# Optimization experiments

Hardware: AMD Instinct MI355X
Metric: run time of the kernel (lower is better)

## Reference

```python
import jax, jax.numpy as jnp
import numpy as np

D_MODEL, SEQ, D_HEAD, N_HEAD, D_MLP = 1024, 2048, 64, 16, 4096
BATCH = 2
LN_EPS = 1e-5


def layer_norm(x, gamma, beta):
    mu = jnp.mean(x, axis=-1, keepdims=True)
    var = jnp.mean(jnp.square(x - mu), axis=-1, keepdims=True)
    return (x - mu) * jax.lax.rsqrt(var + LN_EPS) * gamma + beta


def setup_inputs() -> dict:
    key = jax.random.key(0)
    ks = jax.random.split(key, 10)
    s = 1.0 / np.sqrt(D_MODEL)
    x = jax.random.normal(ks[0], (BATCH, SEQ, D_MODEL), dtype=jnp.float32)
    # per-head Q/K/V projections, stacked: [H, d_model, d_head]
    wq = jax.random.uniform(ks[1], (N_HEAD, D_MODEL, D_HEAD), jnp.float32, -s, s)
    wk = jax.random.uniform(ks[2], (N_HEAD, D_MODEL, D_HEAD), jnp.float32, -s, s)
    wv = jax.random.uniform(ks[3], (N_HEAD, D_MODEL, D_HEAD), jnp.float32, -s, s)
    wo = jax.random.uniform(ks[4], (N_HEAD * D_HEAD, D_MODEL), jnp.float32, -s, s)
    sm = 1.0 / np.sqrt(D_MLP)
    w_in = jax.random.uniform(ks[5], (D_MODEL, D_MLP), jnp.float32, -s, s)
    b_in = jax.random.uniform(ks[6], (D_MLP,), jnp.float32, -s, s)
    w_out = jax.random.uniform(ks[7], (D_MLP, D_MODEL), jnp.float32, -sm, sm)
    b_out = jax.random.uniform(ks[8], (D_MODEL,), jnp.float32, -sm, sm)
    g1 = jnp.ones((D_MODEL,), jnp.float32)
    bt1 = jnp.zeros((D_MODEL,), jnp.float32)
    g2 = jnp.ones((D_MODEL,), jnp.float32)
    bt2 = jnp.zeros((D_MODEL,), jnp.float32)
    return {"x": x, "wq": wq, "wk": wk, "wv": wv, "wo": wo,
            "w_in": w_in, "b_in": b_in, "w_out": w_out, "b_out": b_out,
            "g1": g1, "bt1": bt1, "g2": g2, "bt2": bt2}


def reference(x, wq, wk, wv, wo, w_in, b_in, w_out, b_out, g1, bt1, g2, bt2):
    B, S, D = x.shape
    # multi-head attention (all heads batched)
    q = jnp.einsum('bsd,hde->bhse', x, wq)  # [B,H,S,dh]
    k = jnp.einsum('bsd,hde->bhse', x, wk)
    v = jnp.einsum('bsd,hde->bhse', x, wv)
    scores = jnp.einsum('bhie,bhje->bhij', q, k) / np.sqrt(D_HEAD)
    causal = jnp.tril(jnp.ones((S, S), dtype=bool))
    scores = jnp.where(causal, scores, -jnp.inf)
    attn = jax.nn.softmax(scores, axis=-1)
    head_out = jnp.einsum('bhij,bhje->bhie', attn, v)  # [B,H,S,dh]
    # concat heads in order (head 0 first) -> [B,S,H*dh]
    head_out = jnp.transpose(head_out, (0, 2, 1, 3)).reshape(B, S, N_HEAD * D_HEAD)
    x = x + layer_norm(head_out @ wo, g1, bt1)
    mlp = jax.nn.relu(x @ w_in + b_in) @ w_out + b_out
    x = x + layer_norm(mlp, g2, bt2)
    return x
```

## Files before the change

### kernel.cpp

```cpp
#include <hip/hip_runtime.h>
#include <hip/hip_bf16.h>
#include <math.h>

#define DM 1024
#define SEQ 2048
#define DH 64
#define NH 16
#define DMLP 4096
#define BATCH 2
#define ROWS (BATCH*SEQ)

typedef __attribute__((ext_vector_type(4))) float f32x4;
typedef __attribute__((ext_vector_type(8))) short bf16x8;

__device__ __forceinline__ void gl2lds16(const __hip_bfloat16* g, __hip_bfloat16* l) {
  __builtin_amdgcn_global_load_lds(
      (const __attribute__((address_space(1))) void*)g,
      (__attribute__((address_space(3))) void*)l, 16, 0, 0);
}

template<int K, int OUT_BF16, int BIAS, int RELU>
__global__ __launch_bounds__(512) void gemm256(
    const __hip_bfloat16* __restrict__ A,
    const __hip_bfloat16* __restrict__ BT,
    float* __restrict__ Cf,
    __hip_bfloat16* __restrict__ Cb,
    const float* __restrict__ bias,
    int N)
{
  constexpr int NT = K / 64;
  __shared__ __align__(16) __hip_bfloat16 As[2][16384];
  __shared__ __align__(16) __hip_bfloat16 Bs[2][16384];
  const int t    = threadIdx.x;
  const int wave = t >> 6;
  const int lane = t & 63;
  const int col  = lane & 15;
  const int quad = lane >> 4;
  const int m0 = blockIdx.x * 256;
  const int n0 = blockIdx.y * 256;
  const int wm = (wave >> 2) * 128;
  const int wn = (wave & 3) * 64;

  const int tr = t >> 3;
  const int tc = (t & 7) ^ (tr & 7);
  const __hip_bfloat16* gA = A  + (size_t)(m0 + tr) * K + tc * 8;
  const __hip_bfloat16* gB = BT + (size_t)(n0 + tr) * K + tc * 8;

  const int sw  = col & 7;
  const int ao0 = ((quad)     ^ sw) * 8;
  const int ao1 = ((4 + quad) ^ sw) * 8;

  f32x4 acc[8][4] = {};

#define STAGE_A(h, u) do {                                                     \
    gl2lds16(gA + (size_t)(h)*128*K + (u)*64,                                  \
             &As[(u)&1][(h)*8192 + wave*512]);                                 \
    gl2lds16(gA + (size_t)(h)*128*K + (u)*64 + (size_t)64*K,                   \
             &As[(u)&1][(h)*8192 + 4096 + wave*512]);                          \
  } while (0)
#define STAGE_B(h, u) do {                                                     \
    gl2lds16(gB + (size_t)(h)*128*K + (u)*64,                                  \
             &Bs[(u)&1][(h)*8192 + wave*512]);                                 \
    gl2lds16(gB + (size_t)(h)*128*K + (u)*64 + (size_t)64*K,                   \
             &Bs[(u)&1][(h)*8192 + 4096 + wave*512]);                          \
  } while (0)
#define LOAD_A(base) do { _Pragma("unroll")                                    \
    for (int i = 0; i < 4; ++i) {                                              \
      af[i][0] = *(const bf16x8*)(pA + (base) + i*1024 + ao0);                 \
      af[i][1] = *(const bf16x8*)(pA + (base) + i*1024 + ao1);                 \
    } } while (0)
#define LOAD_BX(arr, base) do { _Pragma("unroll")                              \
    for (int j = 0; j < 2; ++j) {                                              \
      arr[j][0] = *(const bf16x8*)(pB + (base) + j*1024 + ao0);                \
      arr[j][1] = *(const bf16x8*)(pB + (base) + j*1024 + ao1);                \
    } } while (0)
#define PHASE_TAIL(MB, NB, BARR) do {                                          \
    asm volatile("s_barrier" ::: "memory");                                    \
    asm volatile("s_waitcnt lgkmcnt(0)" ::: "memory");                         \
    __builtin_amdgcn_s_setprio(1);                                             \
    _Pragma("unroll")                                                          \
    for (int kk = 0; kk < 2; ++kk)                                             \
      _Pragma("unroll")                                                        \
      for (int i = 0; i < 4; ++i)                                              \
        _Pragma("unroll")                                                      \
        for (int j = 0; j < 2; ++j)                                            \
          acc[(MB)+i][(NB)+j] = __builtin_amdgcn_mfma_f32_16x16x32_bf16(       \
              af[i][kk], BARR[j][kk], acc[(MB)+i][(NB)+j], 0, 0, 0);           \
    __builtin_amdgcn_s_setprio(0);                                             \
    asm volatile("s_barrier" ::: "memory");                                    \
  } while (0)

  STAGE_A(0, 0); STAGE_B(0, 0); STAGE_A(1, 0); STAGE_B(1, 0);
  if (NT > 1) {
    STAGE_A(0, 1); STAGE_B(0, 1); STAGE_A(1, 1); STAGE_B(1, 1);
    asm volatile("s_waitcnt vmcnt(8)" ::: "memory");
  } else {
    asm volatile("s_waitcnt vmcnt(0)" ::: "memory");
  }
  asm volatile("s_barrier" ::: "memory");

  #pragma unroll 2
  for (int u = 0; u < NT; ++u) {
    const __hip_bfloat16* pA = As[u & 1] + (wm + col) * 64;
    const __hip_bfloat16* pB = Bs[u & 1] + (wn + col) * 64;
    const bool s2 = (u + 2 < NT);
    bf16x8 af[4][2], bl[2][2], bh[2][2];

    LOAD_A(0);
    LOAD_BX(bl, 0);
    PHASE_TAIL(0, 0, bl);

    LOAD_BX(bh, 2048);
    PHASE_TAIL(0, 2, bh);

    LOAD_A(4096);
    if (s2) { STAGE_B(0, u + 2); STAGE_B(1, u + 2); }
    PHASE_TAIL(4, 2, bh);

    if (s2) {
      STAGE_A(0, u + 2); STAGE_A(1, u + 2);
      asm volatile("s_waitcnt vmcnt(8)" ::: "memory");
    } else {
      asm volatile("s_waitcnt vmcnt(0)" ::: "memory");
    }
    PHASE_TAIL(4, 0, bl);
  }
#undef STAGE_A
#undef STAGE_B
#undef LOAD_A
#undef LOAD_BX
#undef PHASE_TAIL

  #pragma unroll
  for (int mi = 0; mi < 8; ++mi) {
    #pragma unroll
    for (int ni = 0; ni < 4; ++ni) {
      const int cn = n0 + wn + ni*16 + col;
      float bv = 0.f;
      if (BIAS) bv = bias[cn];
      #pragma unroll
      for (int r = 0; r < 4; ++r) {
        const int cm = m0 + wm + mi*16 + quad*4 + r;
        float v = acc[mi][ni][r];
        if (BIAS) v += bv;
        if (RELU) v = fmaxf(v, 0.f);
        if (OUT_BF16) Cb[(size_t)cm * N + cn] = __float2bfloat16(v);
        else          Cf[(size_t)cm * N + cn] = v;
      }
    }
  }
}

template<int KS>
__global__ __launch_bounds__(512) void gemm256x128(
    const __hip_bfloat16* __restrict__ A,
    const __hip_bfloat16* __restrict__ BT,
    float* __restrict__ Cf,
    int N, int K, long long zstride)
{
  constexpr int NT = KS / 64;
  static_assert(NT >= 2, "pipeline needs >=2 K-tiles");
  __shared__ __align__(16) __hip_bfloat16 As[2][16384];
  __shared__ __align__(16) __hip_bfloat16 Bs[2][8192];
  const int t    = threadIdx.x;
  const int wave = t >> 6;
  const int lane = t & 63;
  const int col  = lane & 15;
  const int quad = lane >> 4;
  const int m0 = blockIdx.x * 256;
  const int n0 = blockIdx.y * 128;
  const int kz = (int)blockIdx.z * KS;
  const int wm = (wave >> 1) * 64;
  const int wn = (wave & 1) * 64;

  const int tr = t >> 3;
  const int tc = (t & 7) ^ (tr & 7);
  const __hip_bfloat16* gA = A  + (size_t)(m0 + tr) * K + kz + tc * 8;
  const __hip_bfloat16* gB = BT + (size_t)(n0 + tr) * K + kz + tc * 8;

  const int sw  = col & 7;
  const int ao0 = ((quad)     ^ sw) * 8;
  const int ao1 = ((4 + quad) ^ sw) * 8;

  f32x4 acc[4][4] = {};

#define SA(u) do { _Pragma("unroll")                                           \
    for (int q = 0; q < 4; ++q)                                                \
      gl2lds16(gA + (size_t)(q*64)*K + (u)*64,                                 \
               &As[(u)&1][q*4096 + wave*512]);                                 \
  } while (0)
#define SB(u) do { _Pragma("unroll")                                           \
    for (int q = 0; q < 2; ++q)                                                \
      gl2lds16(gB + (size_t)(q*64)*K + (u)*64,                                 \
               &Bs[(u)&1][q*4096 + wave*512]);                                 \
  } while (0)

  SA(0); SB(0); SA(1);

  #pragma unroll 2
  for (int v = 0; v < NT; ++v) {
    const __hip_bfloat16* pA = As[v & 1] + (wm + col) * 64;
    const __hip_bfloat16* pB = Bs[v & 1] + (wn + col) * 64;
    bf16x8 af[4][2], bf[4][2];

    if (v + 1 < NT) {
      SB(v + 1);
      asm volatile("s_waitcnt vmcnt(6)" ::: "memory");
    } else {
      asm volatile("s_waitcnt vmcnt(0)" ::: "memory");
    }
    asm volatile("s_barrier" ::: "memory");
    #pragma unroll
    for (int i = 0; i < 4; ++i) {
      af[i][0] = *(const bf16x8*)(pA + i*1024 + ao0);
      af[i][1] = *(const bf16x8*)(pA + i*1024 + ao1);
    }
    #pragma unroll
    for (int j = 0; j < 2; ++j) {
      bf[j][0] = *(const bf16x8*)(pB + j*1024 + ao0);
      bf[j][1] = *(const bf16x8*)(pB + j*1024 + ao1);
    }
    asm volatile("s_waitcnt lgkmcnt(0)" ::: "memory");
    __builtin_amdgcn_s_setprio(1);
    #pragma unroll
    for (int kk = 0; kk < 2; ++kk)
      #pragma unroll
      for (int i = 0; i < 4; ++i)
        #pragma unroll
        for (int j = 0; j < 2; ++j)
          acc[i][j] = __builtin_amdgcn_mfma_f32_16x16x32_bf16(
              af[i][kk], bf[j][kk], acc[i][j], 0, 0, 0);
    __builtin_amdgcn_s_setprio(0);
    asm volatile("s_barrier" ::: "memory");

    if (v + 2 < NT) SA(v + 2);
    #pragma unroll
    for (int j = 2; j < 4; ++j) {
      bf[j][0] = *(const bf16x8*)(pB + j*1024 + ao0);
      bf[j][1] = *(const bf16x8*)(pB + j*1024 + ao1);
    }
    asm volatile("s_waitcnt lgkmcnt(0)" ::: "memory");
    __builtin_amdgcn_s_setprio(1);
    #pragma unroll
    for (int kk = 0; kk < 2; ++kk)
      #pragma unroll
      for (int i = 0; i < 4; ++i)
        #pragma unroll
        for (int j = 2; j < 4; ++j)
          acc[i][j] = __builtin_amdgcn_mfma_f32_16x16x32_bf16(
              af[i][kk], bf[j][kk], acc[i][j], 0, 0, 0);
    __builtin_amdgcn_s_setprio(0);
    asm volatile("s_barrier" ::: "memory");
  }
#undef SA
#undef SB

  float* Co = Cf + (size_t)blockIdx.z * zstride;
  #pragma unroll
  for (int i = 0; i < 4; ++i) {
    #pragma unroll
    for (int j = 0; j < 4; ++j) {
      const int cn = n0 + wn + j*16 + col;
      #pragma unroll
      for (int r = 0; r < 4; ++r) {
        const int cm = m0 + wm + i*16 + quad*4 + r;
        Co[(size_t)cm * N + cn] = acc[i][j][r];
      }
    }
  }
}

__global__ __launch_bounds__(256) void attn_kernel(
    const __hip_bfloat16* __restrict__ qkv,
    const __hip_bfloat16* __restrict__ vt,
    __hip_bfloat16* __restrict__ aout)
{
  __shared__ __align__(16) __hip_bfloat16 Ks[2][64*64];
  __shared__ __align__(16) __hip_bfloat16 Vts[64*64];
  __shared__ __align__(16) __hip_bfloat16 Ps[4][16*64];

  const int bh = blockIdx.x, b = bh >> 4, h = bh & 15;
  const int t = threadIdx.x, wave = t >> 6, lane = t & 63;
  const int col = lane & 15, quad = lane >> 4;
  const float SC = 0.125f * 1.44269504f;

  const int r0  = t >> 3;
  const int cs0 = (t & 7) ^ (r0 & 7);
  const __hip_bfloat16* kbase = qkv + (size_t)b*SEQ*3072 + 1024 + h*64;
  const __hip_bfloat16* vbase = vt + (size_t)bh*64*SEQ;

#define KISSUE(j0, buf) do {                                                      \
    gl2lds16(kbase + (size_t)((j0) + r0)*3072      + cs0*8, &Ks[buf][wave*512]);  \
    gl2lds16(kbase + (size_t)((j0) + 32 + r0)*3072 + cs0*8, &Ks[buf][2048 + wave*512]); \
  } while (0)
#define VISSUE(j0) do {                                                           \
    gl2lds16(vbase + (size_t)r0*SEQ        + (j0) + cs0*8,  &Vts[wave*512]);      \
    gl2lds16(vbase + (size_t)(32 + r0)*SEQ + (j0) + cs0*8,  &Vts[2048 + wave*512]); \
  } while (0)

  const int yq = (int)blockIdx.y >> 3, yr = (int)blockIdx.y & 7;
  const int tile = (yq << 3) | ((yq & 1) ? (7 - yr) : yr);
  const int i0 = tile * 64;
  const int i0w = i0 + wave*16;

  bf16x8 aq[2];
  #pragma unroll
  for (int kk = 0; kk < 2; kk++)
    aq[kk] = *(const bf16x8*)&qkv[((size_t)(b*SEQ + i0w + col))*3072 + h*64 + kk*32 + quad*8];

  f32x4 O[4] = {};
  float lsum[4] = {0.f, 0.f, 0.f, 0.f};

  const int njt = tile + 1;
  KISSUE(0, 0);
  for (int jt = 0; jt < njt; jt++) {
    const int cur = jt & 1;
    const int j0 = jt * 64;
    const bool pf = (jt + 1 < njt);
    asm volatile("s_barrier" ::: "memory");
    VISSUE(j0);
    if (pf) {
      KISSUE(j0 + 64, cur ^ 1);
      asm volatile("s_waitcnt vmcnt(4)" ::: "memory");
    } else {
      asm volatile("s_waitcnt vmcnt(2)" ::: "memory");
    }

    f32x4 S[4] = {};
    __builtin_amdgcn_s_setprio(1);
    #pragma unroll
    for (int kk = 0; kk < 2; kk++) {
      const int sl = ((kk*4 + quad) ^ (col & 7)) * 8;
      #pragma unroll
      for (int jl = 0; jl < 4; jl++) {
        bf16x8 bk = *(const bf16x8*)&Ks[cur][(jl*16 + col)*64 + sl];
        S[jl] = __builtin_amdgcn_mfma_f32_16x16x32_bf16(aq[kk], bk, S[jl], 0, 0, 0);
      }
    }
    __builtin_amdgcn_s_setprio(0);

    const bool diag = (jt == tile);
    #pragma unroll
    for (int r = 0; r < 4; r++) {
      const int row = quad*4 + r;
      const int ig = i0 + wave*16 + row;
      #pragma unroll
      for (int jl = 0; jl < 4; jl++) {
        float p = exp2f(S[jl][r] * SC);
        if (diag && (j0 + jl*16 + col > ig)) p = 0.f;
        lsum[r] += p;
        const int c = jl*2 + (col >> 3);
        Ps[wave][row*64 + (c ^ (row & 7))*8 + (col & 7)] = __float2bfloat16(p);
      }
    }

    if (pf) asm volatile("s_waitcnt vmcnt(2)" ::: "memory");
    else    asm volatile("s_waitcnt vmcnt(0)" ::: "memory");

    __builtin_amdgcn_s_setprio(1);
    #pragma unroll
    for (int kk = 0; kk < 2; kk++) {
      const int sl = ((kk*4 + quad) ^ (col & 7)) * 8;
      bf16x8 ap = *(const bf16x8*)&Ps[wave][col*64 + sl];
      #pragma unroll
      for (int et = 0; et < 4; et++) {
        bf16x8 bv = *(const bf16x8*)&Vts[(et*16 + col)*64 + sl];
        O[et] = __builtin_amdgcn_mfma_f32_16x16x32_bf16(ap, bv, O[et], 0, 0, 0);
      }
    }
    __builtin_amdgcn_s_setprio(0);
  }

  #pragma unroll
  for (int r = 0; r < 4; r++) {
    float s = lsum[r];
    s += __shfl_xor(s, 1);
    s += __shfl_xor(s, 2);
    s += __shfl_xor(s, 4);
    s += __shfl_xor(s, 8);
    const float inv = 1.f / s;
    const int m = b*SEQ + i0w + quad*4 + r;
    #pragma unroll
    for (int et = 0; et < 4; et++)
      aout[(size_t)m*DM + h*64 + et*16 + col] = __float2bfloat16(O[et][r] * inv);
  }
#undef KISSUE
#undef VISSUE
}

__global__ __launch_bounds__(256) void ln_res(
    const float* __restrict__ y0,
    const float* __restrict__ y1,
    const float* __restrict__ bias,
    const float* __restrict__ xres,
    float* __restrict__ xout,
    __hip_bfloat16* __restrict__ bout,
    const float* __restrict__ gamma,
    const float* __restrict__ beta)
{
  const int row = blockIdx.x;
  const int t = threadIdx.x;
  float4 v = ((const float4*)(y0 + (size_t)row*DM))[t];
  if (y1) {
    const float4 w = ((const float4*)(y1 + (size_t)row*DM))[t];
    v.x += w.x; v.y += w.y; v.z += w.z; v.w += w.w;
  }
  if (bias) {
    const float4 w = ((const float4*)bias)[t];
    v.x += w.x; v.y += w.y; v.z += w.z; v.w += w.w;
  }
  float s  = v.x + v.y + v.z + v.w;
  float sq = v.x*v.x + v.y*v.y + v.z*v.z + v.w*v.w;
  #pragma unroll
  for (int off = 32; off > 0; off >>= 1) {
    s  += __shfl_down(s, off);
    sq += __shfl_down(sq, off);
  }
  __shared__ float red[8];
  const int wave = t >> 6, lane = t & 63;
  if (lane == 0) { red[wave] = s; red[4 + wave] = sq; }
  __syncthreads();
  s  = red[0] + red[1] + red[2] + red[3];
  sq = red[4] + red[5] + red[6] + red[7];
  const float mu   = s * (1.f/DM);
  const float var  = sq * (1.f/DM) - mu*mu;
  const float rstd = rsqrtf(var + 1e-5f);
  const float4 g  = ((const float4*)gamma)[t];
  const float4 bt = ((const float4*)beta)[t];
  const float4 xr = ((const float4*)(xres + (size_t)row*DM))[t];
  float4 o;
  o.x = (v.x - mu)*rstd*g.x + bt.x + xr.x;
  o.y = (v.y - mu)*rstd*g.y + bt.y + xr.y;
  o.z = (v.z - mu)*rstd*g.z + bt.z + xr.z;
  o.w = (v.w - mu)*rstd*g.w + bt.w + xr.w;
  ((float4*)(xout + (size_t)row*DM))[t] = o;
  if (bout) {
    __hip_bfloat16* bp = bout + (size_t)row*DM + t*4;
    bp[0] = __float2bfloat16(o.x);
    bp[1] = __float2bfloat16(o.y);
    bp[2] = __float2bfloat16(o.z);
    bp[3] = __float2bfloat16(o.w);
  }
}

__global__ __launch_bounds__(256) void transpose_cvt(
    const float* __restrict__ src, __hip_bfloat16* __restrict__ dst,
    int K, int N, long long sz, long long dz)
{
  __shared__ float tile[32][33];
  const int z = blockIdx.z;
  const int k0 = blockIdx.y * 32, n0 = blockIdx.x * 32;
  const int tx = threadIdx.x & 31, ty = threadIdx.x >> 5;
  const float* s = src + (size_t)z*sz;
  __hip_bfloat16* d = dst + (size_t)z*dz;
  for (int i = ty; i < 32; i += 8)
    tile[i][tx] = s[(size_t)(k0+i)*N + n0 + tx];
  __syncthreads();
  for (int i = ty; i < 32; i += 8)
    d[(size_t)(n0+i)*K + k0 + tx] = __float2bfloat16(tile[tx][i]);
}

__global__ __launch_bounds__(256) void transpose_v(
    const __hip_bfloat16* __restrict__ qkv, __hip_bfloat16* __restrict__ vt)
{
  __shared__ __hip_bfloat16 tile[32][33];
  const int bh = blockIdx.z, b = bh >> 4, h = bh & 15;
  const int s0 = blockIdx.x * 32, e0 = blockIdx.y * 32;
  const int tx = threadIdx.x & 31, ty = threadIdx.x >> 5;
  for (int i = ty; i < 32; i += 8)
    tile[i][tx] = qkv[(size_t)(b*SEQ + s0+i)*3072 + 2048 + h*64 + e0 + tx];
  __syncthreads();
  for (int i = ty; i < 32; i += 8)
    vt[((size_t)bh*64 + e0+i)*SEQ + s0 + tx] = tile[tx][i];
}

__global__ __launch_bounds__(256) void cvt_bf16(
    const float* __restrict__ src, __hip_bfloat16* __restrict__ dst, int n4)
{
  const int i = blockIdx.x*256 + threadIdx.x;
  if (i < n4) {
    const float4 v = ((const float4*)src)[i];
    dst[i*4+0] = __float2bfloat16(v.x);
    dst[i*4+1] = __float2bfloat16(v.y);
    dst[i*4+2] = __float2bfloat16(v.z);
    dst[i*4+3] = __float2bfloat16(v.w);
  }
}

extern "C" void kernel_launch(void* const* d_in, const int* in_sizes, int n_in,
                              void* d_out, int out_size, void* d_ws, size_t ws_size,
                              hipStream_t stream)
{
  const float* x     = (const float*)d_in[0];
  const float* wq    = (const float*)d_in[1];
  const float* wk    = (const float*)d_in[2];
  const float* wv    = (const float*)d_in[3];
  const float* wo    = (const float*)d_in[4];
  const float* w_in  = (const float*)d_in[5];
  const float* b_in  = (const float*)d_in[6];
  const float* w_out = (const float*)d_in[7];
  const float* b_out = (const float*)d_in[8];
  const float* g1    = (const float*)d_in[9];
  const float* bt1   = (const float*)d_in[10];
  const float* g2    = (const float*)d_in[11];
  const float* bt2   = (const float*)d_in[12];
  float* out = (float*)d_out;

  char* ws = (char*)d_ws;
  __hip_bfloat16* xb     = (__hip_bfloat16*)(ws + 0);
  __hip_bfloat16* wqkvT  = (__hip_bfloat16*)(ws + 8388608);
  __hip_bfloat16* woT    = (__hip_bfloat16*)(ws + 14680064);
  __hip_bfloat16* w_inT  = (__hip_bfloat16*)(ws + 16777216);
  __hip_bfloat16* w_outT = (__hip_bfloat16*)(ws + 25165824);
  __hip_bfloat16* qkvb   = (__hip_bfloat16*)(ws + 33554432);
  __hip_bfloat16* vtb    = (__hip_bfloat16*)(ws + 58720256);
  __hip_bfloat16* attn_o = (__hip_bfloat16*)(ws + 67108864);
  float*          P0     = (float*)(ws + 33554432);
  float*          x1     = (float*)(ws + 75497472);
  __hip_bfloat16* x1b    = (__hip_bfloat16*)(ws + 92274688);
  __hip_bfloat16* hbuf   = (__hip_bfloat16*)(ws + 33554432);
  float*          M0     = (float*)(ws + 0);
  float*          M1     = (float*)(ws + 100663296);
  float*          P1     = (float*)(ws + 50331648);

  const long long PROJ_ZS = (long long)ROWS * DM;
  const long long MLP_ZS  = 100663296LL / 4;

  cvt_bf16<<<ROWS*DM/4/256, 256, 0, stream>>>(x, xb, ROWS*DM/4);

  transpose_cvt<<<dim3(2,32,16), 256, 0, stream>>>(wq, wqkvT,             DM, DH, (long long)DM*DH, (long long)DH*DM);
  transpose_cvt<<<dim3(2,32,16), 256, 0, stream>>>(wk, wqkvT + 1024*1024, DM, DH, (long long)DM*DH, (long long)DH*DM);
  transpose_cvt<<<dim3(2,32,16), 256, 0, stream>>>(wv, wqkvT + 2048*1024, DM, DH, (long long)DM*DH, (long long)DH*DM);
  transpose_cvt<<<dim3(32,32,1),  256, 0, stream>>>(wo,    woT,    DM,   DM,   0, 0);
  transpose_cvt<<<dim3(128,32,1), 256, 0, stream>>>(w_in,  w_inT,  DM,   DMLP, 0, 0);
  transpose_cvt<<<dim3(32,128,1), 256, 0, stream>>>(w_out, w_outT, DMLP, DM,   0, 0);

  gemm256<DM,1,0,0><<<dim3(ROWS/256, 3072/256), 512, 0, stream>>>(xb, wqkvT, nullptr, qkvb, nullptr, 3072);
  transpose_v<<<dim3(SEQ/32, 2, BATCH*NH), 256, 0, stream>>>(qkvb, vtb);
  attn_kernel<<<dim3(BATCH*NH, SEQ/64), 256, 0, stream>>>(qkvb, vtb, attn_o);
  gemm256x128<512><<<dim3(ROWS/256, DM/128, 2), 512, 0, stream>>>(attn_o, woT, P0, DM, DM, PROJ_ZS);
  ln_res<<<ROWS, 256, 0, stream>>>(P0, P1, nullptr, x, x1, x1b, g1, bt1);
  gemm256<DM,1,1,1><<<dim3(ROWS/256, DMLP/256), 512, 0, stream>>>(x1b, w_inT, nullptr, hbuf, b_in, DMLP);
  gemm256x128<2048><<<dim3(ROWS/256, DM/128, 2), 512, 0, stream>>>(hbuf, w_outT, M0, DM, DMLP, MLP_ZS);
  ln_res<<<ROWS, 256, 0, stream>>>(M0, M1, b_out, x1, out, nullptr, g2, bt2);
}
```

Before: 233.4 us.

## Split causal attention key range into chunks with separate finalize kernel

Each query tile's causal key range is split into chunks of up to 8 key tiles, so the attention grid grows from 32 to 80 blocks per head and the longest block does bounded work. Tiles beyond the first chunk write unnormalized bf16 partial outputs and row sums to workspace. A new finalize kernel sums the partials and normalizes. The goal is better load balance and occupancy across CUs, at the cost of an extra launch, partial-buffer traffic, and some bf16 rounding of the partials.

```diff
diff --git a/kernel.cpp b/kernel.cpp
--- a/kernel.cpp
+++ b/kernel.cpp
@@ -17,6 +17,12 @@
   __builtin_amdgcn_global_load_lds(
       (const __attribute__((address_space(1))) void*)g,
       (__attribute__((address_space(3))) void*)l, 16, 0, 0);
+}
+
+__device__ __forceinline__ float bfu2f(unsigned short u) {
+  union { unsigned int i; float f; } cvt;
+  cvt.i = ((unsigned int)u) << 16;
+  return cvt.f;
 }
 
 template<int K, int OUT_BF16, int BIAS, int RELU>
@@ -273,7 +279,9 @@
 __global__ __launch_bounds__(256) void attn_kernel(
     const __hip_bfloat16* __restrict__ qkv,
     const __hip_bfloat16* __restrict__ vt,
-    __hip_bfloat16* __restrict__ aout)
+    __hip_bfloat16* __restrict__ aout,
+    __hip_bfloat16* __restrict__ opart,
+    float* __restrict__ lpart)
 {
   __shared__ __align__(16) __hip_bfloat16 Ks[2][64*64];
   __shared__ __align__(16) __hip_bfloat16 Vts[64*64];
@@ -298,8 +306,15 @@
     gl2lds16(vbase + (size_t)(32 + r0)*SEQ + (j0) + cs0*8,  &Vts[2048 + wave*512]); \
   } while (0)
 
-  const int yq = (int)blockIdx.y >> 3, yr = (int)blockIdx.y & 7;
-  const int tile = (yq << 3) | ((yq & 1) ? (7 - yr) : yr);
+  const int y = (int)blockIdx.y;
+  int c, tile;
+  if (y < 32)      { c = 0; tile = 31 - y;  }
+  else if (y < 56) { c = 1; tile = 63 - y;  }
+  else if (y < 72) { c = 2; tile = 87 - y;  }
+  else             { c = 3; tile = 103 - y; }
+  const int jbeg = c * 8;
+  const int jend = jbeg + min(8, tile + 1 - jbeg);
+
   const int i0 = tile * 64;
   const int i0w = i0 + wave*16;
 
@@ -311,12 +326,11 @@
   f32x4 O[4] = {};
   float lsum[4] = {0.f, 0.f, 0.f, 0.f};
 
-  const int njt = tile + 1;
-  KISSUE(0, 0);
-  for (int jt = 0; jt < njt; jt++) {
-    const int cur = jt & 1;
+  KISSUE(jbeg * 64, 0);
+  for (int jt = jbeg; jt < jend; jt++) {
+    const int cur = (jt - jbeg) & 1;
     const int j0 = jt * 64;
-    const bool pf = (jt + 1 < njt);
+    const bool pf = (jt + 1 < jend);
     asm volatile("s_barrier" ::: "memory");
     VISSUE(j0);
     if (pf) {
@@ -349,8 +363,8 @@
         float p = exp2f(S[jl][r] * SC);
         if (diag && (j0 + jl*16 + col > ig)) p = 0.f;
         lsum[r] += p;
-        const int c = jl*2 + (col >> 3);
-        Ps[wave][row*64 + (c ^ (row & 7))*8 + (col & 7)] = __float2bfloat16(p);
+        const int cc = jl*2 + (col >> 3);
+        Ps[wave][row*64 + (cc ^ (row & 7))*8 + (col & 7)] = __float2bfloat16(p);
       }
     }
 
@@ -378,14 +392,50 @@
     s += __shfl_xor(s, 2);
     s += __shfl_xor(s, 4);
     s += __shfl_xor(s, 8);
-    const float inv = 1.f / s;
     const int m = b*SEQ + i0w + quad*4 + r;
-    #pragma unroll
-    for (int et = 0; et < 4; et++)
-      aout[(size_t)m*DM + h*64 + et*16 + col] = __float2bfloat16(O[et][r] * inv);
+    if (tile < 8) {
+      const float inv = 1.f / s;
+      #pragma unroll
+      for (int et = 0; et < 4; et++)
+        aout[(size_t)m*DM + h*64 + et*16 + col] = __float2bfloat16(O[et][r] * inv);
+    } else {
+      __hip_bfloat16* op = opart + ((size_t)c*ROWS + m)*DM + h*64;
+      #pragma unroll
+      for (int et = 0; et < 4; et++)
+        op[et*16 + col] = __float2bfloat16(O[et][r]);
+      if (col == 0) lpart[((size_t)c*ROWS + m)*16 + h] = s;
+    }
   }
 #undef KISSUE
 #undef VISSUE
+}
+
+__global__ __launch_bounds__(256) void attn_finalize(
+    const __hip_bfloat16* __restrict__ opart,
+    const float* __restrict__ lpart,
+    __hip_bfloat16* __restrict__ aout)
+{
+  const int y = blockIdx.x;
+  const int b = y / 1536;
+  const int rem = y % 1536;
+  const int tile = 8 + (rem >> 6);
+  const int rr = rem & 63;
+  const int m = b*SEQ + tile*64 + rr;
+  const int nch = (tile >> 3) + 1;
+  const int tid = threadIdx.x;
+  const int h = tid >> 4;
+  float o0 = 0.f, o1 = 0.f, o2 = 0.f, o3 = 0.f, l = 0.f;
+  for (int c = 0; c < nch; ++c) {
+    const ushort4 v = ((const ushort4*)(opart + ((size_t)c*ROWS + m)*DM))[tid];
+    o0 += bfu2f(v.x); o1 += bfu2f(v.y); o2 += bfu2f(v.z); o3 += bfu2f(v.w);
+    l  += lpart[((size_t)c*ROWS + m)*16 + h];
+  }
+  const float inv = 1.f / l;
+  __hip_bfloat16* p = aout + (size_t)m*DM + tid*4;
+  p[0] = __float2bfloat16(o0 * inv);
+  p[1] = __float2bfloat16(o1 * inv);
+  p[2] = __float2bfloat16(o2 * inv);
+  p[3] = __float2bfloat16(o3 * inv);
 }
 
 __global__ __launch_bounds__(256) void ln_res(
@@ -514,7 +564,9 @@
   __hip_bfloat16* w_outT = (__hip_bfloat16*)(ws + 25165824);
   __hip_bfloat16* qkvb   = (__hip_bfloat16*)(ws + 33554432);
   __hip_bfloat16* vtb    = (__hip_bfloat16*)(ws + 58720256);
-  __hip_bfloat16* attn_o = (__hip_bfloat16*)(ws + 67108864);
+  __hip_bfloat16* attn_o = (__hip_bfloat16*)(ws + 0);
+  __hip_bfloat16* opart  = (__hip_bfloat16*)(ws + 67108864);
+  float*          lpart  = (float*)(ws + 100663296);
   float*          P0     = (float*)(ws + 33554432);
   float*          x1     = (float*)(ws + 75497472);
   __hip_bfloat16* x1b    = (__hip_bfloat16*)(ws + 92274688);
@@ -537,7 +589,8 @@
 
   gemm256<DM,1,0,0><<<dim3(ROWS/256, 3072/256), 512, 0, stream>>>(xb, wqkvT, nullptr, qkvb, nullptr, 3072);
   transpose_v<<<dim3(SEQ/32, 2, BATCH*NH), 256, 0, stream>>>(qkvb, vtb);
-  attn_kernel<<<dim3(BATCH*NH, SEQ/64), 256, 0, stream>>>(qkvb, vtb, attn_o);
+  attn_kernel<<<dim3(BATCH*NH, 80), 256, 0, stream>>>(qkvb, vtb, attn_o, opart, lpart);
+  attn_finalize<<<3072, 256, 0, stream>>>(opart, lpart, attn_o);
   gemm256x128<512><<<dim3(ROWS/256, DM/128, 2), 512, 0, stream>>>(attn_o, woT, P0, DM, DM, PROJ_ZS);
   ln_res<<<ROWS, 256, 0, stream>>>(P0, P1, nullptr, x, x1, x1b, g1, bt1);
   gemm256<DM,1,1,1><<<dim3(ROWS/256, DMLP/256), 512, 0, stream>>>(x1b, w_inT, nullptr, hbuf, b_in, DMLP);
```

After: 238.0 us. 1.02x slower.
